# Optimization experiments

Hardware: AMD Instinct MI355X
Metric: run time of the kernel (lower is better)

## Reference

```python
import jax, jax.numpy as jnp
import numpy as np

COMMITMENT = 0.25
THRESHOLD = 0.6
SNR_DB = 30.0  # eval_snr_db default-ish channel condition (fixed for determinism)
LN_EPS = 1e-5


def _layernorm(x, g, b):
    m = jnp.mean(x, axis=-1, keepdims=True)
    v = jnp.var(x, axis=-1, keepdims=True)
    return (x - m) * jax.lax.rsqrt(v + LN_EPS) * g + b


def _vq(x, codebook):
    # x: [T, D], codebook: [K, D]. Nearest-neighbor quantize + per-token VQ loss + STE.
    d = (x * x).sum(-1, keepdims=True) - 2.0 * (x @ codebook.T) + (codebook * codebook).sum(-1)  # [T, K]
    idx = jnp.argmin(d, axis=-1)
    q = codebook[idx]  # [T, D]
    loss = (COMMITMENT * jnp.mean((x - jax.lax.stop_gradient(q)) ** 2, axis=-1)
            + jnp.mean((jax.lax.stop_gradient(x) - q) ** 2, axis=-1))  # [T]
    q_ste = x + jax.lax.stop_gradient(q - x)
    return q_ste, loss


def setup_inputs() -> dict:
    key = jax.random.key(0)
    ks = jax.random.split(key, 8)
    B, N, De, Dq, Dd = 64, 196, 768, 512, 256
    return {
        'x_tokens': jax.random.normal(ks[0], (B, N, De), jnp.float32),
        'fim_logits': jax.random.normal(ks[1], (B, N, 1), jnp.float32),
        'W_proj': jax.random.normal(ks[2], (De, Dq), jnp.float32) * (1.0 / np.sqrt(De)),
        'b_proj': jnp.zeros((Dq,), jnp.float32),
        'ln_g': jnp.ones((Dq,), jnp.float32),
        'ln_b': jnp.zeros((Dq,), jnp.float32),
        'cb_high': jax.random.normal(ks[3], (4096, Dq), jnp.float32),
        'cb_low': jax.random.normal(ks[4], (256, Dq), jnp.float32),
        'W_dec': jax.random.normal(ks[5], (Dq, Dd), jnp.float32) * (1.0 / np.sqrt(Dq)),
        'b_dec': jnp.zeros((Dd,), jnp.float32),
        'h_ri': jax.random.normal(ks[6], (B, 2), jnp.float32),
        'noise': jax.random.normal(ks[7], (B, N, Dq), jnp.float32),
    }


def reference(x_tokens, fim_logits, W_proj, b_proj, ln_g, ln_b, cb_high, cb_low, W_dec, b_dec, h_ri, noise):
    B, N, _ = x_tokens.shape
    score = jax.nn.sigmoid(fim_logits[..., 0])          # [B, N]
    route_high = score > THRESHOLD                       # [B, N] bool

    x_proj = _layernorm(x_tokens @ W_proj + b_proj, ln_g, ln_b)  # [B, N, Dq]
    D = x_proj.shape[-1]
    xf = x_proj.reshape(-1, D)
    mf = route_high.reshape(-1)
    sf = score.reshape(-1)

    # Compute both experts densely, select with mask (same math as the masked
    # gather/scatter dispatch in the torch code, jit-friendly static shapes).
    q_high, loss_high = _vq(xf, cb_high)
    q_low, loss_low = _vq(xf, cb_low)
    final = jnp.where(mf[:, None], q_high, q_low).reshape(B, N, D)

    n_high = jnp.maximum(mf.sum(), 1)
    n_low = jnp.maximum((~mf).sum(), 1)
    vq_loss = (jnp.sum(jnp.where(mf, loss_high * sf, 0.0)) / n_high
               + jnp.sum(jnp.where(mf, 0.0, loss_low * (1.0 - sf))) / n_low) / 2.0

    # Rayleigh channel: per-sample fading magnitude h = |CN(0,1)|/sqrt(2), AWGN, equalize.
    n_var = 10.0 ** (-SNR_DB / 10.0)
    h = jnp.sqrt((h_ri ** 2).sum(-1)) / jnp.sqrt(2.0)    # [B]
    h = h[:, None, None]
    y = (h * final + jnp.sqrt(n_var) * noise) / h

    x_dec = y @ W_dec + b_dec                            # [B, N, 256]
    return x_dec, vq_loss
```

## Files before the change

kernel.cpp:

```cpp
#include <hip/hip_runtime.h>
#include <math.h>

#define T_TOK 12544
#define DE 768
#define DQ 512
#define DD 256
#define SEQ 196
#define NCH 4096
#define NCL 256
#define SPL_H 16
#define CODES_PER_BLK 256
#define MARGIN 2.0f
#define CAND_CAP 16
#define VQTOK 128

typedef __attribute__((ext_vector_type(8))) short s16x8;
typedef __attribute__((ext_vector_type(4))) float f32x4;

__device__ __forceinline__ float wave_reduce_sum(float v) {
    #pragma unroll
    for (int off = 32; off > 0; off >>= 1) v += __shfl_xor(v, off);
    return v;
}

__device__ __forceinline__ unsigned short f2bf(float f) {
    unsigned int u = __float_as_uint(f);
    u = (u + 0x7fffu + ((u >> 16) & 1u)) >> 16;
    return (unsigned short)u;
}
__device__ __forceinline__ float bf2f(unsigned short h) {
    return __uint_as_float(((unsigned int)h) << 16);
}

__device__ __forceinline__ void gload_lds16(const unsigned short* g, unsigned short* l) {
    __builtin_amdgcn_global_load_lds(
        (const __attribute__((address_space(1))) void*)g,
        (__attribute__((address_space(3))) void*)l,
        16, 0, 0);
}

__device__ __forceinline__ void sumsq_body(const float* __restrict__ cb,
                                           float* __restrict__ cs2,
                                           unsigned short* __restrict__ cbB,
                                           int blk, int NC) {
    int row = blk * 4 + (threadIdx.x >> 6);
    int lane = threadIdx.x & 63;
    if (row >= NC) return;
    const float4* p = (const float4*)(cb + (size_t)row * DQ);
    float4 a = p[lane];
    float4 b = p[lane + 64];
    if (cbB) {
        unsigned short* dst = cbB + (size_t)row * DQ;
        ushort4 ha, hb;
        ha.x = f2bf(a.x); ha.y = f2bf(a.y); ha.z = f2bf(a.z); ha.w = f2bf(a.w);
        hb.x = f2bf(b.x); hb.y = f2bf(b.y); hb.z = f2bf(b.z); hb.w = f2bf(b.w);
        *(ushort4*)(dst + lane * 4) = ha;
        *(ushort4*)(dst + 256 + lane * 4) = hb;
    }
    float s = a.x*a.x + a.y*a.y + a.z*a.z + a.w*a.w
            + b.x*b.x + b.y*b.y + b.z*b.z + b.w*b.w;
    s = wave_reduce_sum(s);
    if (lane == 0) cs2[row] = s;
}

__device__ __forceinline__ void split_body(const float* __restrict__ W, int K, int N,
                                           unsigned short* __restrict__ Thi,
                                           unsigned short* __restrict__ Tlo,
                                           int blk, int nb) {
    int total = K * N;
    for (int idx = blk * 256 + threadIdx.x; idx < total; idx += nb * 256) {
        int n = idx / K, k = idx - n * K;
        float v = W[(size_t)k * N + n];
        unsigned short h = f2bf(v);
        Thi[idx] = h;
        Tlo[idx] = f2bf(v - bf2f(h));
    }
}

__global__ __launch_bounds__(256) void prep_all(const float* __restrict__ cb_h,
                                                float* __restrict__ cs2h,
                                                unsigned short* __restrict__ cbhB,
                                                const float* __restrict__ cb_l,
                                                float* __restrict__ cs2l,
                                                unsigned short* __restrict__ cblB,
                                                const float* __restrict__ Wp,
                                                unsigned short* __restrict__ WThi,
                                                unsigned short* __restrict__ WTlo,
                                                const float* __restrict__ Wd,
                                                unsigned short* __restrict__ WdThi,
                                                unsigned short* __restrict__ WdTlo,
                                                int* __restrict__ counts) {
    int blk = blockIdx.x;
    if (blk == 0 && threadIdx.x == 0) { counts[0] = 0; counts[1] = 0; }
    if (blk < 1024)       sumsq_body(cb_h, cs2h, cbhB, blk, NCH);
    else if (blk < 1088)  sumsq_body(cb_l, cs2l, cblB, blk - 1024, NCL);
    else if (blk < 1600)  split_body(Wp, DE, DQ, WThi, WTlo, blk - 1088, 512);
    else                  split_body(Wd, DQ, DD, WdThi, WdTlo, blk - 1600, 256);
}

template<int NC>
__global__ __launch_bounds__(256) void code_sumsq(const float* __restrict__ cb,
                                                  float* __restrict__ cs2) {
    sumsq_body(cb, cs2, nullptr, blockIdx.x, NC);
}

template<int KDIM, int NSTRIDE>
__global__ __launch_bounds__(256) void gemm_mfma3_128(const float* __restrict__ A,
                                                      const unsigned short* __restrict__ BThi,
                                                      const unsigned short* __restrict__ BTlo,
                                                      const float* __restrict__ bias,
                                                      float* __restrict__ out) {
    __shared__ __align__(16) unsigned short Ahi[128 * 32];
    __shared__ __align__(16) unsigned short Alo[128 * 32];
    __shared__ __align__(16) unsigned short Bhi[128 * 32];
    __shared__ __align__(16) unsigned short Blo[128 * 32];
    const int m0 = blockIdx.x * 128, n0 = blockIdx.y * 128;
    const int tid = threadIdx.x, lane = tid & 63, w = tid >> 6;
    const int wr = w >> 1, wc = w & 1;
    const int arow = tid >> 1, ahalf = tid & 1;

    const int cb0 = w * 2, cb1 = w * 2 + 1;
    const int gcol0 = n0 + cb0 * 16 + (lane >> 2);
    const int gcol1 = n0 + cb1 * 16 + (lane >> 2);
    const int ch0 = (lane & 3) ^ ((gcol0 >> 1) & 3);
    const int ch1 = (lane & 3) ^ ((gcol1 >> 1) & 3);
    const unsigned short* sH0 = BThi + (size_t)gcol0 * KDIM + ch0 * 8;
    const unsigned short* sH1 = BThi + (size_t)gcol1 * KDIM + ch1 * 8;
    const unsigned short* sL0 = BTlo + (size_t)gcol0 * KDIM + ch0 * 8;
    const unsigned short* sL1 = BTlo + (size_t)gcol1 * KDIM + ch1 * 8;

    f32x4 acc[4][4] = {};
    const int NT = KDIM / 32;
    for (int t = 0; t < NT; t++) {
        const int k0 = t * 32;
        gload_lds16(sH0 + k0, Bhi + cb0 * 512);
        gload_lds16(sH1 + k0, Bhi + cb1 * 512);
        gload_lds16(sL0 + k0, Blo + cb0 * 512);
        gload_lds16(sL1 + k0, Blo + cb1 * 512);
        {
            const float* src = A + (size_t)(m0 + arow) * KDIM + k0 + ahalf * 16;
            float4 v0 = *(const float4*)(src + 0);
            float4 v1 = *(const float4*)(src + 4);
            float4 v2 = *(const float4*)(src + 8);
            float4 v3 = *(const float4*)(src + 12);
            float xv[16] = {v0.x,v0.y,v0.z,v0.w, v1.x,v1.y,v1.z,v1.w,
                            v2.x,v2.y,v2.z,v2.w, v3.x,v3.y,v3.z,v3.w};
            const int swzA = (arow >> 1) & 3;
            #pragma unroll
            for (int cc = 0; cc < 2; cc++) {
                unsigned int hw[4], lw[4];
                #pragma unroll
                for (int j = 0; j < 4; j++) {
                    float f0 = xv[cc*8 + 2*j], f1 = xv[cc*8 + 2*j + 1];
                    unsigned short h0 = f2bf(f0), h1 = f2bf(f1);
                    unsigned short l0 = f2bf(f0 - bf2f(h0));
                    unsigned short l1 = f2bf(f1 - bf2f(h1));
                    hw[j] = (unsigned)h0 | ((unsigned)h1 << 16);
                    lw[j] = (unsigned)l0 | ((unsigned)l1 << 16);
                }
                int c = ahalf * 2 + cc;
                int doff = arow * 32 + (c ^ swzA) * 8;
                *(uint4*)&Ahi[doff] = make_uint4(hw[0], hw[1], hw[2], hw[3]);
                *(uint4*)&Alo[doff] = make_uint4(lw[0], lw[1], lw[2], lw[3]);
            }
        }
        __syncthreads();
        const int fr = lane & 15, fs = lane >> 4;
        s16x8 ah[4], al[4];
        #pragma unroll
        for (int tm = 0; tm < 4; tm++) {
            int row = wr * 64 + tm * 16 + fr;
            int off = row * 32 + (fs ^ ((row >> 1) & 3)) * 8;
            ah[tm] = *(const s16x8*)&Ahi[off];
            al[tm] = *(const s16x8*)&Alo[off];
        }
        #pragma unroll
        for (int tn = 0; tn < 4; tn++) {
            int col = wc * 64 + tn * 16 + fr;
            int boff = col * 32 + (fs ^ ((col >> 1) & 3)) * 8;
            s16x8 bh = *(const s16x8*)&Bhi[boff];
            s16x8 bl = *(const s16x8*)&Blo[boff];
            #pragma unroll
            for (int tm = 0; tm < 4; tm++) {
                acc[tm][tn] = __builtin_amdgcn_mfma_f32_16x16x32_bf16(ah[tm], bh, acc[tm][tn], 0, 0, 0);
                acc[tm][tn] = __builtin_amdgcn_mfma_f32_16x16x32_bf16(ah[tm], bl, acc[tm][tn], 0, 0, 0);
                acc[tm][tn] = __builtin_amdgcn_mfma_f32_16x16x32_bf16(al[tm], bh, acc[tm][tn], 0, 0, 0);
            }
        }
        __syncthreads();
    }
    const int fr = lane & 15, fg = lane >> 4;
    #pragma unroll
    for (int tn = 0; tn < 4; tn++) {
        const int col = n0 + wc * 64 + tn * 16 + fr;
        const float bb = bias[col];
        #pragma unroll
        for (int tm = 0; tm < 4; tm++) {
            #pragma unroll
            for (int r = 0; r < 4; r++) {
                int row = m0 + wr * 64 + tm * 16 + fg * 4 + r;
                out[(size_t)row * NSTRIDE + col] = acc[tm][tn][r] + bb;
            }
        }
    }
}

__global__ __launch_bounds__(256) void dec_mfma3_loss(const float* __restrict__ A,
                                                      const unsigned short* __restrict__ BThi,
                                                      const unsigned short* __restrict__ BTlo,
                                                      const float* __restrict__ bias,
                                                      float* __restrict__ out,
                                                      const float* __restrict__ lh,
                                                      const float* __restrict__ ll,
                                                      const int* __restrict__ counts) {
    __shared__ __align__(16) unsigned short Ahi[2][64 * 32];
    __shared__ __align__(16) unsigned short Alo[2][64 * 32];
    __shared__ __align__(16) unsigned short Bhi[2][64 * 32];
    __shared__ __align__(16) unsigned short Blo[2][64 * 32];
    if (blockIdx.x == T_TOK / 64) {
        if (blockIdx.y != 0) return;
        float* sh = (float*)&Ahi[0][0];
        float* sl = sh + 256;
        int tid = threadIdx.x;
        float ah = 0.f, al = 0.f;
        for (int t = tid; t < T_TOK; t += 256) { ah += lh[t]; al += ll[t]; }
        sh[tid] = ah; sl[tid] = al;
        __syncthreads();
        for (int o = 128; o > 0; o >>= 1) {
            if (tid < o) { sh[tid] += sh[tid + o]; sl[tid] += sl[tid + o]; }
            __syncthreads();
        }
        if (tid == 0) {
            int nh = counts[0];
            int nl = T_TOK - nh;
            nh = nh > 1 ? nh : 1;
            nl = nl > 1 ? nl : 1;
            out[(size_t)T_TOK * DD] = 0.5f * (sh[0] / (float)nh + sl[0] / (float)nl);
        }
        return;
    }
    const int m0 = blockIdx.x * 64, n0 = blockIdx.y * 64;
    const int tid = threadIdx.x, lane = tid & 63, w = tid >> 6;
    const int stok = tid >> 2, sslot = tid & 3;

    f32x4 acc[4] = {};
    float4 av0, av1;
    uint4 bh4, bl4;

    auto loadStep = [&](int k0) {
        const float* src = A + (size_t)(m0 + stok) * DQ + k0 + sslot * 8;
        av0 = *(const float4*)src;
        av1 = *(const float4*)(src + 4);
        size_t soff = (size_t)(n0 + stok) * DQ + k0 + sslot * 8;
        bh4 = *(const uint4*)(BThi + soff);
        bl4 = *(const uint4*)(BTlo + soff);
    };
    auto writeStep = [&](int buf) {
        float xv[8] = {av0.x, av0.y, av0.z, av0.w, av1.x, av1.y, av1.z, av1.w};
        unsigned int hw[4], lw[4];
        #pragma unroll
        for (int j = 0; j < 4; j++) {
            unsigned short h0 = f2bf(xv[2*j]),   h1 = f2bf(xv[2*j+1]);
            unsigned short l0 = f2bf(xv[2*j] - bf2f(h0));
            unsigned short l1 = f2bf(xv[2*j+1] - bf2f(h1));
            hw[j] = (unsigned)h0 | ((unsigned)h1 << 16);
            lw[j] = (unsigned)l0 | ((unsigned)l1 << 16);
        }
        int doffA = stok * 32 + (sslot ^ ((stok >> 1) & 3)) * 8;
        *(uint4*)&Ahi[buf][doffA] = make_uint4(hw[0], hw[1], hw[2], hw[3]);
        *(uint4*)&Alo[buf][doffA] = make_uint4(lw[0], lw[1], lw[2], lw[3]);
        *(uint4*)&Bhi[buf][doffA] = bh4;
        *(uint4*)&Blo[buf][doffA] = bl4;
    };

    loadStep(0); writeStep(0); __syncthreads();
    const int NT = DQ / 32;
    for (int t = 0; t < NT; t++) {
        const int cur = t & 1;
        if (t + 1 < NT) loadStep((t + 1) * 32);
        const int fr = lane & 15, fs = lane >> 4;
        s16x8 ah[4], al[4];
        #pragma unroll
        for (int tm = 0; tm < 4; tm++) {
            int tok = tm * 16 + fr;
            int off = tok * 32 + (fs ^ ((tok >> 1) & 3)) * 8;
            ah[tm] = *(const s16x8*)&Ahi[cur][off];
            al[tm] = *(const s16x8*)&Alo[cur][off];
        }
        {
            int col = w * 16 + fr;
            int boff = col * 32 + (fs ^ ((col >> 1) & 3)) * 8;
            s16x8 bh = *(const s16x8*)&Bhi[cur][boff];
            s16x8 bl = *(const s16x8*)&Blo[cur][boff];
            #pragma unroll
            for (int tm = 0; tm < 4; tm++) {
                acc[tm] = __builtin_amdgcn_mfma_f32_16x16x32_bf16(ah[tm], bh, acc[tm], 0, 0, 0);
                acc[tm] = __builtin_amdgcn_mfma_f32_16x16x32_bf16(ah[tm], bl, acc[tm], 0, 0, 0);
                acc[tm] = __builtin_amdgcn_mfma_f32_16x16x32_bf16(al[tm], bh, acc[tm], 0, 0, 0);
            }
        }
        if (t + 1 < NT) writeStep(cur ^ 1);
        __syncthreads();
    }
    const int fr = lane & 15, fg = lane >> 4;
    {
        const int col = n0 + w * 16 + fr;
        const float bb = bias[col];
        #pragma unroll
        for (int tm = 0; tm < 4; tm++) {
            #pragma unroll
            for (int r = 0; r < 4; r++) {
                int row = m0 + tm * 16 + fg * 4 + r;
                out[(size_t)row * DD + col] = acc[tm][r] + bb;
            }
        }
    }
}

__global__ __launch_bounds__(256) void proj_gemm(const float* __restrict__ X,
                                                 const float* __restrict__ W,
                                                 const float* __restrict__ bias,
                                                 float* __restrict__ out) {
    __shared__ float As[32][66];
    __shared__ float Bs[32][64];
    const int m0 = blockIdx.x * 64, n0 = blockIdx.y * 64;
    const int tid = threadIdx.x;
    const int tx = tid & 15, ty = tid >> 4;
    float acc[4][4] = {};
    for (int k0 = 0; k0 < DE; k0 += 32) {
        {
            int e = tid;
            int r = e >> 3, c4 = e & 7;
            float4 v = *(const float4*)(X + (size_t)(m0 + r) * DE + k0 + c4 * 4);
            As[c4*4+0][r] = v.x; As[c4*4+1][r] = v.y; As[c4*4+2][r] = v.z; As[c4*4+3][r] = v.w;
            e = tid + 256;
            r = e >> 3; c4 = e & 7;
            v = *(const float4*)(X + (size_t)(m0 + r) * DE + k0 + c4 * 4);
            As[c4*4+0][r] = v.x; As[c4*4+1][r] = v.y; As[c4*4+2][r] = v.z; As[c4*4+3][r] = v.w;
        }
        {
            int e = tid;
            int kk = e >> 4, c4 = e & 15;
            *(float4*)&Bs[kk][c4*4] = *(const float4*)(W + (size_t)(k0 + kk) * DQ + n0 + c4 * 4);
            e = tid + 256;
            kk = e >> 4; c4 = e & 15;
            *(float4*)&Bs[kk][c4*4] = *(const float4*)(W + (size_t)(k0 + kk) * DQ + n0 + c4 * 4);
        }
        __syncthreads();
        #pragma unroll
        for (int k = 0; k < 32; k++) {
            float2 a01 = *(const float2*)&As[k][ty * 4];
            float2 a23 = *(const float2*)&As[k][ty * 4 + 2];
            float4 b = *(const float4*)&Bs[k][tx * 4];
            float av[4] = {a01.x, a01.y, a23.x, a23.y};
            float bv[4] = {b.x, b.y, b.z, b.w};
            #pragma unroll
            for (int i = 0; i < 4; i++)
                #pragma unroll
                for (int j = 0; j < 4; j++)
                    acc[i][j] += av[i] * bv[j];
        }
        __syncthreads();
    }
    float4 bv4 = *(const float4*)(bias + n0 + tx * 4);
    float bb[4] = {bv4.x, bv4.y, bv4.z, bv4.w};
    #pragma unroll
    for (int i = 0; i < 4; i++) {
        int row = m0 + ty * 4 + i;
        float4 o;
        o.x = acc[i][0] + bb[0];
        o.y = acc[i][1] + bb[1];
        o.z = acc[i][2] + bb[2];
        o.w = acc[i][3] + bb[3];
        *(float4*)(out + (size_t)row * DQ + n0 + tx * 4) = o;
    }
}

__global__ __launch_bounds__(256) void ln_route_compact(float* __restrict__ xp,
                                                        const float* __restrict__ g,
                                                        const float* __restrict__ b,
                                                        const float* __restrict__ logits,
                                                        float* __restrict__ score,
                                                        unsigned short* __restrict__ xpB,
                                                        int* __restrict__ hlist,
                                                        int* __restrict__ llist,
                                                        int* __restrict__ counts) {
    __shared__ int hloc[32], lloc[32];
    __shared__ int nh_s, nl_s, bh_s, bl_s;
    const int tid = threadIdx.x, lane = tid & 63, wv = tid >> 6;
    if (tid == 0) { nh_s = 0; nl_s = 0; }
    __syncthreads();
    float4 g0 = *(const float4*)(g + lane * 4);
    float4 g1 = *(const float4*)(g + 256 + lane * 4);
    float4 b0 = *(const float4*)(b + lane * 4);
    float4 b1 = *(const float4*)(b + 256 + lane * 4);
    const int rbase = blockIdx.x * 32 + wv * 8;
    for (int i = 0; i < 8; i++) {
        int row = rbase + i;
        float* p = xp + (size_t)row * DQ;
        float4 v0 = *(float4*)(p + lane * 4);
        float4 v1 = *(float4*)(p + 256 + lane * 4);
        float s  = v0.x + v0.y + v0.z + v0.w + v1.x + v1.y + v1.z + v1.w;
        float ss = v0.x*v0.x + v0.y*v0.y + v0.z*v0.z + v0.w*v0.w
                 + v1.x*v1.x + v1.y*v1.y + v1.z*v1.z + v1.w*v1.w;
        s = wave_reduce_sum(s);
        ss = wave_reduce_sum(ss);
        float m = s * (1.f / DQ);
        float var = ss * (1.f / DQ) - m * m;
        float scale = rsqrtf(var + 1e-5f);
        float4 o0, o1;
        o0.x = (v0.x - m) * scale * g0.x + b0.x;
        o0.y = (v0.y - m) * scale * g0.y + b0.y;
        o0.z = (v0.z - m) * scale * g0.z + b0.z;
        o0.w = (v0.w - m) * scale * g0.w + b0.w;
        o1.x = (v1.x - m) * scale * g1.x + b1.x;
        o1.y = (v1.y - m) * scale * g1.y + b1.y;
        o1.z = (v1.z - m) * scale * g1.z + b1.z;
        o1.w = (v1.w - m) * scale * g1.w + b1.w;
        *(float4*)(p + lane * 4) = o0;
        *(float4*)(p + 256 + lane * 4) = o1;
        unsigned short* dst = xpB + (size_t)row * DQ;
        ushort4 h0, h1;
        h0.x = f2bf(o0.x); h0.y = f2bf(o0.y); h0.z = f2bf(o0.z); h0.w = f2bf(o0.w);
        h1.x = f2bf(o1.x); h1.y = f2bf(o1.y); h1.z = f2bf(o1.z); h1.w = f2bf(o1.w);
        *(ushort4*)(dst + lane * 4) = h0;
        *(ushort4*)(dst + 256 + lane * 4) = h1;
        if (lane == 0) {
            float lg = logits[row];
            float sc = 1.f / (1.f + expf(-lg));
            score[row] = sc;
            if (sc > 0.6f) { int pp = atomicAdd(&nh_s, 1); hloc[pp] = row; }
            else           { int pp = atomicAdd(&nl_s, 1); lloc[pp] = row; }
        }
    }
    __syncthreads();
    if (tid == 0) {
        bh_s = atomicAdd(&counts[0], nh_s);
        bl_s = atomicAdd(&counts[1], nl_s);
    }
    __syncthreads();
    if (tid < 32) {
        if (tid < nh_s) hlist[bh_s + tid] = hloc[tid];
    } else if (tid < 64) {
        int j = tid - 32;
        if (j < nl_s) llist[bl_s + j] = lloc[j];
    }
}

__global__ __launch_bounds__(256) void ln_route(float* __restrict__ xp,
                                                const float* __restrict__ g,
                                                const float* __restrict__ b,
                                                const float* __restrict__ logits,
                                                float* __restrict__ score,
                                                int* __restrict__ mask,
                                                unsigned short* __restrict__ xpB) {
    int row = blockIdx.x * 4 + (threadIdx.x >> 6);
    int lane = threadIdx.x & 63;
    float* p = xp + (size_t)row * DQ;
    float4 v0 = *(float4*)(p + lane * 4);
    float4 v1 = *(float4*)(p + 256 + lane * 4);
    float s  = v0.x + v0.y + v0.z + v0.w + v1.x + v1.y + v1.z + v1.w;
    float ss = v0.x*v0.x + v0.y*v0.y + v0.z*v0.z + v0.w*v0.w
             + v1.x*v1.x + v1.y*v1.y + v1.z*v1.z + v1.w*v1.w;
    s = wave_reduce_sum(s);
    ss = wave_reduce_sum(ss);
    float m = s * (1.f / DQ);
    float var = ss * (1.f / DQ) - m * m;
    float scale = rsqrtf(var + 1e-5f);
    float4 g0 = *(const float4*)(g + lane * 4);
    float4 g1 = *(const float4*)(g + 256 + lane * 4);
    float4 b0 = *(const float4*)(b + lane * 4);
    float4 b1 = *(const float4*)(b + 256 + lane * 4);
    float4 o0, o1;
    o0.x = (v0.x - m) * scale * g0.x + b0.x;
    o0.y = (v0.y - m) * scale * g0.y + b0.y;
    o0.z = (v0.z - m) * scale * g0.z + b0.z;
    o0.w = (v0.w - m) * scale * g0.w + b0.w;
    o1.x = (v1.x - m) * scale * g1.x + b1.x;
    o1.y = (v1.y - m) * scale * g1.y + b1.y;
    o1.z = (v1.z - m) * scale * g1.z + b1.z;
    o1.w = (v1.w - m) * scale * g1.w + b1.w;
    *(float4*)(p + lane * 4) = o0;
    *(float4*)(p + 256 + lane * 4) = o1;
    if (xpB) {
        unsigned short* dst = xpB + (size_t)row * DQ;
        ushort4 h0, h1;
        h0.x = f2bf(o0.x); h0.y = f2bf(o0.y); h0.z = f2bf(o0.z); h0.w = f2bf(o0.w);
        h1.x = f2bf(o1.x); h1.y = f2bf(o1.y); h1.z = f2bf(o1.z); h1.w = f2bf(o1.w);
        *(ushort4*)(dst + lane * 4) = h0;
        *(ushort4*)(dst + 256 + lane * 4) = h1;
    }
    if (lane == 0) {
        float lg = logits[row];
        float sc = 1.f / (1.f + expf(-lg));
        score[row] = sc;
        mask[row] = sc > 0.6f ? 1 : 0;
    }
}

__global__ __launch_bounds__(1024) void scan_compact(const int* __restrict__ mask,
                                                     int* __restrict__ hlist,
                                                     int* __restrict__ llist,
                                                     int* __restrict__ counts) {
    __shared__ int wsum[16];
    __shared__ int base_h, base_l;
    int tid = threadIdx.x, lane = tid & 63, wid = tid >> 6;
    if (tid == 0) { base_h = 0; base_l = 0; }
    __syncthreads();
    for (int t0 = 0; t0 < T_TOK; t0 += 1024) {
        int t = t0 + tid;
        int valid = t < T_TOK;
        int m = valid ? mask[t] : 0;
        unsigned long long bal = __ballot(m);
        int pre = __popcll(bal & ((1ull << lane) - 1ull));
        if (lane == 0) wsum[wid] = __popcll(bal);
        __syncthreads();
        int woff = 0;
        for (int w = 0; w < wid; w++) woff += wsum[w];
        int btot = 0;
        for (int w = 0; w < 16; w++) btot += wsum[w];
        int vcnt = T_TOK - t0; if (vcnt > 1024) vcnt = 1024;
        int bh = base_h, bl = base_l;
        if (valid) {
            if (m) hlist[bh + woff + pre] = t;
            else   llist[bl + (tid - (woff + pre))] = t;
        }
        __syncthreads();
        if (tid == 0) { base_h = bh + btot; base_l = bl + (vcnt - btot); }
        __syncthreads();
    }
    if (tid == 0) { counts[0] = base_h; counts[1] = base_l; }
}

__global__ __launch_bounds__(512) void vq_mfma_all(const unsigned short* __restrict__ xpB,
                                                   const unsigned short* __restrict__ cbhB,
                                                   const float* __restrict__ cs2h,
                                                   const int* __restrict__ hlist,
                                                   const unsigned short* __restrict__ cblB,
                                                   const float* __restrict__ cs2l,
                                                   const int* __restrict__ llist,
                                                   const int* __restrict__ counts,
                                                   float* __restrict__ smaxH,
                                                   int* __restrict__ scntH,
                                                   uint2* __restrict__ candH,
                                                   float* __restrict__ smaxL,
                                                   int* __restrict__ scntL,
                                                   uint2* __restrict__ candL) {
    const int by = blockIdx.y;
    const unsigned short* cbB; const float* cs2; const int* list;
    float* smax; int* scnt; uint2* cand;
    int count, slice, SPLIT;
    if (by < SPL_H) {
        cbB = cbhB; cs2 = cs2h; list = hlist; count = counts[0];
        slice = by; SPLIT = SPL_H; smax = smaxH; scnt = scntH; cand = candH;
    } else {
        cbB = cblB; cs2 = cs2l; list = llist; count = counts[1];
        slice = 0; SPLIT = 1; smax = smaxL; scnt = scntL; cand = candL;
    }
    const int base = blockIdx.x * VQTOK;
    if (base >= count) return;
    const int cbase = slice * CODES_PER_BLK;

    __shared__ __align__(16) unsigned short Abuf[VQTOK * 32];
    __shared__ __align__(16) unsigned short Bbuf[256 * 32];
    __shared__ float wmaxs[8][64];
    __shared__ float tokmax[VQTOK];
    __shared__ int ccnt[VQTOK];
    __shared__ uint2 cland[VQTOK][CAND_CAP];
    __shared__ int rows_s[VQTOK];

    const int tid = threadIdx.x;
    const int lane = tid & 63;
    const int w = tid >> 6;
    const int wr = w >> 2, wc = w & 3;
    const int stok = tid >> 2, sslot = tid & 3;

    if (tid < VQTOK) {
        int tl = base + tid;
        rows_s[tid] = list[tl < count ? tl : (count - 1)];
        ccnt[tid] = 0;
    }
    __syncthreads();

    const int swz = sslot ^ ((stok >> 1) & 3);
    const unsigned short* gA  = xpB + (size_t)rows_s[stok] * DQ + swz * 8;
    const unsigned short* gB0 = cbB + (size_t)(cbase + stok) * DQ + swz * 8;
    const unsigned short* gB1 = cbB + (size_t)(cbase + 128 + stok) * DQ + swz * 8;
    unsigned short* dA  = Abuf + w * 512;
    unsigned short* dB0 = Bbuf + w * 512;
    unsigned short* dB1 = Bbuf + 128 * 32 + w * 512;

    f32x4 acc[4][4] = {};

    const int NT = DQ / 32;
    for (int t = 0; t < NT; t++) {
        const int k0 = t * 32;
        gload_lds16(gA  + k0, dA);
        gload_lds16(gB0 + k0, dB0);
        gload_lds16(gB1 + k0, dB1);
        __syncthreads();
        const int fr = lane & 15, fs = lane >> 4;
        s16x8 af[4], bf[4];
        #pragma unroll
        for (int tm = 0; tm < 4; tm++) {
            int tok = wr * 64 + tm * 16 + fr;
            af[tm] = *(const s16x8*)&Abuf[tok * 32 + (fs ^ ((tok >> 1) & 3)) * 8];
        }
        #pragma unroll
        for (int tn = 0; tn < 4; tn++) {
            int cl = wc * 64 + tn * 16 + fr;
            bf[tn] = *(const s16x8*)&Bbuf[cl * 32 + (fs ^ ((cl >> 1) & 3)) * 8];
        }
        #pragma unroll
        for (int tm = 0; tm < 4; tm++)
            #pragma unroll
            for (int tn = 0; tn < 4; tn++)
                acc[tm][tn] = __builtin_amdgcn_mfma_f32_16x16x32_bf16(af[tm], bf[tn], acc[tm][tn], 0, 0, 0);
        __syncthreads();
    }

    const int fr = lane & 15, fg = lane >> 4;
    float c2[4];
    #pragma unroll
    for (int tn = 0; tn < 4; tn++) c2[tn] = 0.5f * cs2[cbase + wc * 64 + tn * 16 + fr];

    #pragma unroll
    for (int tm = 0; tm < 4; tm++) {
        #pragma unroll
        for (int r = 0; r < 4; r++) {
            float m4 = -3.0e38f;
            #pragma unroll
            for (int tn = 0; tn < 4; tn++) {
                float s = acc[tm][tn][r] - c2[tn];
                m4 = fmaxf(m4, s);
            }
            #pragma unroll
            for (int off = 1; off < 16; off <<= 1)
                m4 = fmaxf(m4, __shfl_xor(m4, off));
            if (fr == 0) wmaxs[w][tm * 16 + fg * 4 + r] = m4;
        }
    }
    __syncthreads();
    if (tid < VQTOK) {
        int wrt = tid >> 6, tlc = tid & 63;
        tokmax[tid] = fmaxf(fmaxf(wmaxs[wrt * 4 + 0][tlc], wmaxs[wrt * 4 + 1][tlc]),
                            fmaxf(wmaxs[wrt * 4 + 2][tlc], wmaxs[wrt * 4 + 3][tlc]));
    }
    __syncthreads();

    #pragma unroll
    for (int tm = 0; tm < 4; tm++) {
        #pragma unroll
        for (int r = 0; r < 4; r++) {
            int token = wr * 64 + tm * 16 + fg * 4 + r;
            float thr = tokmax[token] - MARGIN;
            #pragma unroll
            for (int tn = 0; tn < 4; tn++) {
                float s = acc[tm][tn][r] - c2[tn];
                if (s > thr) {
                    int pos = atomicAdd(&ccnt[token], 1);
                    if (pos < CAND_CAP) {
                        uint2 cd;
                        cd.x = __float_as_uint(s);
                        cd.y = (unsigned)(cbase + wc * 64 + tn * 16 + fr);
                        cland[token][pos] = cd;
                    }
                }
            }
        }
    }
    __syncthreads();

    if (tid < VQTOK) {
        int tl = base + tid;
        if (tl < count) {
            smax[(size_t)tl * SPLIT + slice] = tokmax[tid];
            scnt[(size_t)tl * SPLIT + slice] = min(ccnt[tid], CAND_CAP);
        }
    }
    for (int i = tid; i < VQTOK * CAND_CAP; i += 512) {
        int token = i >> 4, j = i & (CAND_CAP - 1);
        int tl = base + token;
        if (tl < count && j < min(ccnt[token], CAND_CAP))
            cand[((size_t)tl * SPLIT + slice) * CAND_CAP + j] = cland[token][j];
    }
}

__global__ __launch_bounds__(256) void vq_rescore_all(float* __restrict__ xp,
                                                      const float* __restrict__ cb_h,
                                                      const float* __restrict__ smaxH,
                                                      const int* __restrict__ scntH,
                                                      const uint2* __restrict__ candH,
                                                      const int* __restrict__ hlist,
                                                      const float* __restrict__ cb_l,
                                                      const float* __restrict__ smaxL,
                                                      const int* __restrict__ scntL,
                                                      const uint2* __restrict__ candL,
                                                      const int* __restrict__ llist,
                                                      const int* __restrict__ counts,
                                                      int* __restrict__ out_idx,
                                                      const float* __restrict__ noise,
                                                      const float* __restrict__ h_ri,
                                                      const float* __restrict__ score,
                                                      float* __restrict__ lh,
                                                      float* __restrict__ ll) {
    const int HB = T_TOK / 4;
    int bx = blockIdx.x;
    const float* cb; const float* smax; const int* scnt; const uint2* cand; const int* list;
    int count, SPLIT, cidx;
    if (bx < HB) {
        cb = cb_h; smax = smaxH; scnt = scntH; cand = candH; list = hlist;
        count = counts[0]; SPLIT = SPL_H; cidx = 0;
    } else {
        bx -= HB;
        cb = cb_l; smax = smaxL; scnt = scntL; cand = candL; list = llist;
        count = counts[1]; SPLIT = 1; cidx = 1;
    }
    const int wid = threadIdx.x >> 6;
    const int lane = threadIdx.x & 63;
    const int tl = bx * 4 + wid;
    if (tl >= count) return;

    float gm = -3.0e38f;
    if (lane < SPLIT) gm = smax[(size_t)tl * SPLIT + lane];
    #pragma unroll
    for (int off = 1; off < 64; off <<= 1)
        gm = fmaxf(gm, __shfl_xor(gm, off));
    const float thr = gm - MARGIN;

    const int t = list[tl];
    float xv[8];
    #pragma unroll
    for (int kk = 0; kk < 8; kk++) xv[kk] = xp[(size_t)t * DQ + lane * 8 + kk];

    double bs = -1.0e300;
    int bi = 0x7fffffff;
    for (int s = 0; s < SPLIT; s++) {
        int cn = scnt[(size_t)tl * SPLIT + s];
        for (int j = 0; j < cn; j++) {
            uint2 cd = cand[((size_t)tl * SPLIT + s) * CAND_CAP + j];
            float av = __uint_as_float(cd.x);
            if (av >= thr) {
                int code = (int)cd.y;
                const float* crow = cb + (size_t)code * DQ;
                double dot = 0.0, nrm = 0.0;
                #pragma unroll
                for (int kk = 0; kk < 8; kk++) {
                    double cv = (double)crow[lane * 8 + kk];
                    dot += (double)xv[kk] * cv;
                    nrm += cv * cv;
                }
                #pragma unroll
                for (int off = 1; off < 64; off <<= 1) {
                    dot += __shfl_xor(dot, off);
                    nrm += __shfl_xor(nrm, off);
                }
                double sc = dot - 0.5 * nrm;
                if (sc > bs || (sc == bs && code < bi)) { bs = sc; bi = code; }
            }
        }
    }
    const float* qrow = cb + (size_t)bi * DQ;
    float4 q0 = *(const float4*)(qrow + lane * 8);
    float4 q1 = *(const float4*)(qrow + lane * 8 + 4);
    const float* nz = noise + (size_t)t * DQ;
    float4 n0 = *(const float4*)(nz + lane * 8);
    float4 n1 = *(const float4*)(nz + lane * 8 + 4);
    float ds = 0.f, dx;
    dx = xv[0] - q0.x; ds += dx * dx;
    dx = xv[1] - q0.y; ds += dx * dx;
    dx = xv[2] - q0.z; ds += dx * dx;
    dx = xv[3] - q0.w; ds += dx * dx;
    dx = xv[4] - q1.x; ds += dx * dx;
    dx = xv[5] - q1.y; ds += dx * dx;
    dx = xv[6] - q1.z; ds += dx * dx;
    dx = xv[7] - q1.w; ds += dx * dx;
    ds = wave_reduce_sum(ds);
    int bbt = t / SEQ;
    float hh0 = h_ri[bbt * 2], hh1 = h_ri[bbt * 2 + 1];
    float hh = sqrtf((hh0 * hh0 + hh1 * hh1) * 0.5f);
    float cc = sqrtf(1e-3f) / hh;
    float4 y0, y1;
    y0.x = q0.x + cc * n0.x; y0.y = q0.y + cc * n0.y;
    y0.z = q0.z + cc * n0.z; y0.w = q0.w + cc * n0.w;
    y1.x = q1.x + cc * n1.x; y1.y = q1.y + cc * n1.y;
    y1.z = q1.z + cc * n1.z; y1.w = q1.w + cc * n1.w;
    *(float4*)(xp + (size_t)t * DQ + lane * 8) = y0;
    *(float4*)(xp + (size_t)t * DQ + lane * 8 + 4) = y1;
    if (lane == 0) {
        out_idx[t] = bi;
        float loss = 1.25f * ds * (1.f / DQ);
        float sc = score[t];
        if (cidx == 0) { lh[t] = loss * sc;  ll[t] = 0.f; }
        else           { lh[t] = 0.f;        ll[t] = loss * (1.f - sc); }
    }
}

template<int NC, int SPLIT>
__global__ __launch_bounds__(256) void vq_partial(const float* __restrict__ xp,
                                                  const float* __restrict__ cb,
                                                  const float* __restrict__ cs2,
                                                  const int* __restrict__ list,
                                                  const int* __restrict__ counts,
                                                  int cidx,
                                                  float* __restrict__ part_s,
                                                  int* __restrict__ part_i) {
    const int count = counts[cidx];
    const int base = blockIdx.x * 64;
    if (base >= count) return;
    const int CODES = NC / SPLIT;
    const int cbase = blockIdx.y * CODES;
    __shared__ float As[32][68];
    __shared__ float Cs[32][68];
    __shared__ int rows_s[64];
    const int tid = threadIdx.x;
    if (tid < 64) {
        int tl = base + tid;
        rows_s[tid] = list[tl < count ? tl : (count - 1)];
    }
    __syncthreads();
    const int tx = tid & 15, ty = tid >> 4;
    float best_s[4];
    int best_i[4];
    #pragma unroll
    for (int i = 0; i < 4; i++) { best_s[i] = -3.0e38f; best_i[i] = 0; }
    for (int c0 = cbase; c0 < cbase + CODES; c0 += 64) {
        float acc[4][4] = {};
        for (int k0 = 0; k0 < DQ; k0 += 32) {
            {
                int e = tid;
                int r = e >> 3, c4 = e & 7;
                float4 v = *(const float4*)(xp + (size_t)rows_s[r] * DQ + k0 + c4 * 4);
                As[c4*4+0][r] = v.x; As[c4*4+1][r] = v.y; As[c4*4+2][r] = v.z; As[c4*4+3][r] = v.w;
                e = tid + 256; r = e >> 3; c4 = e & 7;
                v = *(const float4*)(xp + (size_t)rows_s[r] * DQ + k0 + c4 * 4);
                As[c4*4+0][r] = v.x; As[c4*4+1][r] = v.y; As[c4*4+2][r] = v.z; As[c4*4+3][r] = v.w;
            }
            {
                int e = tid;
                int r = e >> 3, c4 = e & 7;
                float4 v = *(const float4*)(cb + (size_t)(c0 + r) * DQ + k0 + c4 * 4);
                Cs[c4*4+0][r] = v.x; Cs[c4*4+1][r] = v.y; Cs[c4*4+2][r] = v.z; Cs[c4*4+3][r] = v.w;
                e = tid + 256; r = e >> 3; c4 = e & 7;
                v = *(const float4*)(cb + (size_t)(c0 + r) * DQ + k0 + c4 * 4);
                Cs[c4*4+0][r] = v.x; Cs[c4*4+1][r] = v.y; Cs[c4*4+2][r] = v.z; Cs[c4*4+3][r] = v.w;
            }
            __syncthreads();
            #pragma unroll
            for (int k = 0; k < 32; k++) {
                float4 a = *(const float4*)&As[k][ty * 4];
                float4 b = *(const float4*)&Cs[k][tx * 4];
                float av[4] = {a.x, a.y, a.z, a.w};
                float bv[4] = {b.x, b.y, b.z, b.w};
                #pragma unroll
                for (int i = 0; i < 4; i++)
                    #pragma unroll
                    for (int j = 0; j < 4; j++)
                        acc[i][j] += av[i] * bv[j];
            }
            __syncthreads();
        }
        float4 c2v = *(const float4*)(cs2 + c0 + tx * 4);
        float c2[4] = {c2v.x, c2v.y, c2v.z, c2v.w};
        #pragma unroll
        for (int i = 0; i < 4; i++) {
            float s = acc[i][0] - 0.5f * c2[0];
            int bi = c0 + tx * 4;
            #pragma unroll
            for (int j = 1; j < 4; j++) {
                float sj = acc[i][j] - 0.5f * c2[j];
                if (sj > s) { s = sj; bi = c0 + tx * 4 + j; }
            }
            #pragma unroll
            for (int off = 1; off < 16; off <<= 1) {
                float os = __shfl_xor(s, off);
                int oi = __shfl_xor(bi, off);
                if (os > s || (os == s && oi < bi)) { s = os; bi = oi; }
            }
            if (s > best_s[i] || (s == best_s[i] && bi < best_i[i])) {
                best_s[i] = s; best_i[i] = bi;
            }
        }
    }
    if (tx == 0) {
        #pragma unroll
        for (int i = 0; i < 4; i++) {
            int tl = base + ty * 4 + i;
            if (tl < count) {
                part_s[(size_t)tl * SPLIT + blockIdx.y] = best_s[i];
                part_i[(size_t)tl * SPLIT + blockIdx.y] = best_i[i];
            }
        }
    }
}

template<int SPLIT>
__global__ __launch_bounds__(256) void vq_reduce(const float* __restrict__ part_s,
                                                 const int* __restrict__ part_i,
                                                 const int* __restrict__ list,
                                                 const int* __restrict__ counts,
                                                 int cidx,
                                                 int* __restrict__ out_idx) {
    int tl = blockIdx.x * 256 + threadIdx.x;
    if (tl >= counts[cidx]) return;
    float bs = part_s[(size_t)tl * SPLIT];
    int bi = part_i[(size_t)tl * SPLIT];
    #pragma unroll
    for (int s = 1; s < SPLIT; s++) {
        float v = part_s[(size_t)tl * SPLIT + s];
        int vi = part_i[(size_t)tl * SPLIT + s];
        if (v > bs || (v == bs && vi < bi)) { bs = v; bi = vi; }
    }
    out_idx[list[tl]] = bi;
}

__global__ __launch_bounds__(256) void gather_loss_y(float* __restrict__ xp,
                                                     const float* __restrict__ cb_h,
                                                     const float* __restrict__ cb_l,
                                                     const int* __restrict__ idx,
                                                     const float* __restrict__ score,
                                                     const int* __restrict__ mask,
                                                     const float* __restrict__ noise,
                                                     const float* __restrict__ h_ri,
                                                     float* __restrict__ lh,
                                                     float* __restrict__ ll) {
    int t = blockIdx.x * 4 + (threadIdx.x >> 6);
    int lane = threadIdx.x & 63;
    int m = mask[t];
    float sc = score[t];
    const float* q = (m ? cb_h : cb_l) + (size_t)idx[t] * DQ;
    float* x = xp + (size_t)t * DQ;
    const float* nz = noise + (size_t)t * DQ;
    int bb = t / SEQ;
    float h0 = h_ri[bb * 2], h1 = h_ri[bb * 2 + 1];
    float h = sqrtf((h0 * h0 + h1 * h1) * 0.5f);
    float c = sqrtf(1e-3f) / h;
    float4 xv0 = *(float4*)(x + lane * 4);
    float4 xv1 = *(float4*)(x + 256 + lane * 4);
    float4 qv0 = *(const float4*)(q + lane * 4);
    float4 qv1 = *(const float4*)(q + 256 + lane * 4);
    float4 nv0 = *(const float4*)(nz + lane * 4);
    float4 nv1 = *(const float4*)(nz + 256 + lane * 4);
    float dx, ds = 0.f;
    dx = xv0.x - qv0.x; ds += dx * dx;
    dx = xv0.y - qv0.y; ds += dx * dx;
    dx = xv0.z - qv0.z; ds += dx * dx;
    dx = xv0.w - qv0.w; ds += dx * dx;
    dx = xv1.x - qv1.x; ds += dx * dx;
    dx = xv1.y - qv1.y; ds += dx * dx;
    dx = xv1.z - qv1.z; ds += dx * dx;
    dx = xv1.w - qv1.w; ds += dx * dx;
    ds = wave_reduce_sum(ds);
    float4 y0, y1;
    y0.x = qv0.x + c * nv0.x; y0.y = qv0.y + c * nv0.y;
    y0.z = qv0.z + c * nv0.z; y0.w = qv0.w + c * nv0.w;
    y1.x = qv1.x + c * nv1.x; y1.y = qv1.y + c * nv1.y;
    y1.z = qv1.z + c * nv1.z; y1.w = qv1.w + c * nv1.w;
    *(float4*)(x + lane * 4) = y0;
    *(float4*)(x + 256 + lane * 4) = y1;
    if (lane == 0) {
        float loss = 1.25f * ds * (1.f / DQ);
        lh[t] = m ? loss * sc : 0.f;
        ll[t] = m ? 0.f : loss * (1.f - sc);
    }
}

__global__ __launch_bounds__(256) void loss_reduce(const float* __restrict__ lh,
                                                   const float* __restrict__ ll,
                                                   const int* __restrict__ counts,
                                                   float* __restrict__ out) {
    __shared__ float sh[256], sl[256];
    int tid = threadIdx.x;
    float ah = 0.f, al = 0.f;
    for (int t = tid; t < T_TOK; t += 256) { ah += lh[t]; al += ll[t]; }
    sh[tid] = ah; sl[tid] = al;
    __syncthreads();
    for (int o = 128; o > 0; o >>= 1) {
        if (tid < o) { sh[tid] += sh[tid + o]; sl[tid] += sl[tid + o]; }
        __syncthreads();
    }
    if (tid == 0) {
        int nh = counts[0];
        int nl = T_TOK - nh;
        nh = nh > 1 ? nh : 1;
        nl = nl > 1 ? nl : 1;
        out[(size_t)T_TOK * DD] = 0.5f * (sh[0] / (float)nh + sl[0] / (float)nl);
    }
}

__global__ __launch_bounds__(256) void dec_gemm(const float* __restrict__ Y,
                                                const float* __restrict__ W,
                                                const float* __restrict__ bias,
                                                float* __restrict__ out) {
    __shared__ float As[32][66];
    __shared__ float Bs[32][64];
    const int m0 = blockIdx.x * 64, n0 = blockIdx.y * 64;
    const int tid = threadIdx.x;
    const int tx = tid & 15, ty = tid >> 4;
    float acc[4][4] = {};
    for (int k0 = 0; k0 < DQ; k0 += 32) {
        {
            int e = tid;
            int r = e >> 3, c4 = e & 7;
            float4 v = *(const float4*)(Y + (size_t)(m0 + r) * DQ + k0 + c4 * 4);
            As[c4*4+0][r] = v.x; As[c4*4+1][r] = v.y; As[c4*4+2][r] = v.z; As[c4*4+3][r] = v.w;
            e = tid + 256; r = e >> 3; c4 = e & 7;
            v = *(const float4*)(Y + (size_t)(m0 + r) * DQ + k0 + c4 * 4);
            As[c4*4+0][r] = v.x; As[c4*4+1][r] = v.y; As[c4*4+2][r] = v.z; As[c4*4+3][r] = v.w;
        }
        {
            int e = tid;
            int kk = e >> 4, c4 = e & 15;
            *(float4*)&Bs[kk][c4*4] = *(const float4*)(W + (size_t)(k0 + kk) * DD + n0 + c4 * 4);
            e = tid + 256; kk = e >> 4; c4 = e & 15;
            *(float4*)&Bs[kk][c4*4] = *(const float4*)(W + (size_t)(k0 + kk) * DD + n0 + c4 * 4);
        }
        __syncthreads();
        #pragma unroll
        for (int k = 0; k < 32; k++) {
            float2 a01 = *(const float2*)&As[k][ty * 4];
            float2 a23 = *(const float2*)&As[k][ty * 4 + 2];
            float4 b = *(const float4*)&Bs[k][tx * 4];
            float av[4] = {a01.x, a01.y, a23.x, a23.y};
            float bv[4] = {b.x, b.y, b.z, b.w};
            #pragma unroll
            for (int i = 0; i < 4; i++)
                #pragma unroll
                for (int j = 0; j < 4; j++)
                    acc[i][j] += av[i] * bv[j];
        }
        __syncthreads();
    }
    float4 bv4 = *(const float4*)(bias + n0 + tx * 4);
    float bbv[4] = {bv4.x, bv4.y, bv4.z, bv4.w};
    #pragma unroll
    for (int i = 0; i < 4; i++) {
        int row = m0 + ty * 4 + i;
        float4 o;
        o.x = acc[i][0] + bbv[0];
        o.y = acc[i][1] + bbv[1];
        o.z = acc[i][2] + bbv[2];
        o.w = acc[i][3] + bbv[3];
        *(float4*)(out + (size_t)row * DD + n0 + tx * 4) = o;
    }
}

extern "C" void kernel_launch(void* const* d_in, const int* in_sizes, int n_in,
                              void* d_out, int out_size, void* d_ws, size_t ws_size,
                              hipStream_t stream) {
    const float* x_tokens = (const float*)d_in[0];
    const float* fim      = (const float*)d_in[1];
    const float* W_proj   = (const float*)d_in[2];
    const float* b_proj   = (const float*)d_in[3];
    const float* ln_g     = (const float*)d_in[4];
    const float* ln_b     = (const float*)d_in[5];
    const float* cb_high  = (const float*)d_in[6];
    const float* cb_low   = (const float*)d_in[7];
    const float* W_dec    = (const float*)d_in[8];
    const float* b_dec    = (const float*)d_in[9];
    const float* h_ri     = (const float*)d_in[10];
    const float* noise    = (const float*)d_in[11];
    float* out = (float*)d_out;

    char* ws = (char*)d_ws;
    size_t off = 0;
    float* xp = (float*)(ws + off);     off += (size_t)T_TOK * DQ * 4;
    int*   idxb = (int*)(ws + off);     off += (size_t)T_TOK * 4;
    float* score = (float*)(ws + off);  off += (size_t)T_TOK * 4;
    int*   mask = (int*)(ws + off);     off += (size_t)T_TOK * 4;
    float* lh = (float*)(ws + off);     off += (size_t)T_TOK * 4;
    float* ll = (float*)(ws + off);     off += (size_t)T_TOK * 4;
    int*   hlist = (int*)(ws + off);    off += (size_t)T_TOK * 4;
    int*   llist = (int*)(ws + off);    off += (size_t)T_TOK * 4;
    int*   counts = (int*)(ws + off);   off += 64;
    float* cs2h = (float*)(ws + off);   off += (size_t)NCH * 4;
    float* cs2l = (float*)(ws + off);   off += (size_t)NCL * 4;
    size_t off_common = off;

    unsigned short* xpB  = (unsigned short*)(ws + off); off += (size_t)T_TOK * DQ * 2;
    unsigned short* cbhB = (unsigned short*)(ws + off); off += (size_t)NCH * DQ * 2;
    unsigned short* cblB = (unsigned short*)(ws + off); off += (size_t)NCL * DQ * 2;
    float* smaxH = (float*)(ws + off);  off += (size_t)T_TOK * SPL_H * 4;
    int*   scntH = (int*)(ws + off);    off += (size_t)T_TOK * SPL_H * 4;
    uint2* candH = (uint2*)(ws + off);  off += (size_t)T_TOK * SPL_H * CAND_CAP * 8;
    float* smaxL = (float*)(ws + off);  off += (size_t)T_TOK * 4;
    int*   scntL = (int*)(ws + off);    off += (size_t)T_TOK * 4;
    uint2* candL = (uint2*)(ws + off);  off += (size_t)T_TOK * CAND_CAP * 8;
    unsigned short* WThi  = (unsigned short*)(ws + off); off += (size_t)DQ * DE * 2;
    unsigned short* WTlo  = (unsigned short*)(ws + off); off += (size_t)DQ * DE * 2;
    unsigned short* WdThi = (unsigned short*)(ws + off); off += (size_t)DD * DQ * 2;
    unsigned short* WdTlo = (unsigned short*)(ws + off); off += (size_t)DD * DQ * 2;
    size_t need_new = off;
    const bool use_mfma = ws_size >= need_new;

    if (use_mfma) {
        prep_all<<<1856, 256, 0, stream>>>(cb_high, cs2h, cbhB, cb_low, cs2l, cblB,
                                           W_proj, WThi, WTlo, W_dec, WdThi, WdTlo, counts);
        gemm_mfma3_128<DE, DQ><<<dim3(T_TOK / 128, DQ / 128), 256, 0, stream>>>(
            x_tokens, WThi, WTlo, b_proj, xp);
        ln_route_compact<<<T_TOK / 32, 256, 0, stream>>>(
            xp, ln_g, ln_b, fim, score, xpB, hlist, llist, counts);
        vq_mfma_all<<<dim3(T_TOK / VQTOK, SPL_H + 1), 512, 0, stream>>>(
            xpB, cbhB, cs2h, hlist, cblB, cs2l, llist, counts,
            smaxH, scntH, candH, smaxL, scntL, candL);
        vq_rescore_all<<<2 * (T_TOK / 4), 256, 0, stream>>>(
            xp, cb_high, smaxH, scntH, candH, hlist,
            cb_low, smaxL, scntL, candL, llist,
            counts, idxb, noise, h_ri, score, lh, ll);
        dec_mfma3_loss<<<dim3(T_TOK / 64 + 1, DD / 64), 256, 0, stream>>>(
            xp, WdThi, WdTlo, b_dec, out, lh, ll, counts);
    } else {
        code_sumsq<NCH><<<NCH / 4, 256, 0, stream>>>(cb_high, cs2h);
        code_sumsq<NCL><<<NCL / 4, 256, 0, stream>>>(cb_low, cs2l);
        proj_gemm<<<dim3(T_TOK / 64, DQ / 64), 256, 0, stream>>>(x_tokens, W_proj, b_proj, xp);
        ln_route<<<T_TOK / 4, 256, 0, stream>>>(xp, ln_g, ln_b, fim, score, mask, nullptr);
        scan_compact<<<1, 1024, 0, stream>>>(mask, hlist, llist, counts);
        float* part_s = (float*)(ws + off_common);
        int*   part_i = (int*)(ws + off_common + (size_t)T_TOK * 16 * 4);
        vq_partial<NCH, 16><<<dim3(T_TOK / 64, 16), 256, 0, stream>>>(
            xp, cb_high, cs2h, hlist, counts, 0, part_s, part_i);
        vq_reduce<16><<<(T_TOK + 255) / 256, 256, 0, stream>>>(part_s, part_i, hlist, counts, 0, idxb);
        vq_partial<NCL, 4><<<dim3(T_TOK / 64, 4), 256, 0, stream>>>(
            xp, cb_low, cs2l, llist, counts, 1, part_s, part_i);
        vq_reduce<4><<<(T_TOK + 255) / 256, 256, 0, stream>>>(part_s, part_i, llist, counts, 1, idxb);
        gather_loss_y<<<T_TOK / 4, 256, 0, stream>>>(xp, cb_high, cb_low, idxb, score, mask,
                                                     noise, h_ri, lh, ll);
        loss_reduce<<<1, 256, 0, stream>>>(lh, ll, counts, out);
        dec_gemm<<<dim3(T_TOK / 64, DD / 64), 256, 0, stream>>>(xp, W_dec, b_dec, out);
    }
}
```

Measured before the change: 198.0 us.

## Triple-buffer VQ distance GEMM with async LDS loads and union shared memory

```diff
diff --git a/kernel.cpp b/kernel.cpp
--- a/kernel.cpp
+++ b/kernel.cpp
@@ -283,7 +283,9 @@
         #pragma unroll
         for (int tm = 0; tm < 4; tm++) {
             int tok = tm * 16 + fr;
-            int off = tok * 32 + (fs ^ ((tok >> 1) & 3)) * 8;
+            int off = tok * 32 + (sslot, fs ^ ((tok >> 1) & 3)) * 8;
+            (void)off;
+            off = tok * 32 + (fs ^ ((tok >> 1) & 3)) * 8;
             ah[tm] = *(const s16x8*)&Ahi[cur][off];
             al[tm] = *(const s16x8*)&Alo[cur][off];
         }
@@ -561,13 +563,12 @@
     if (base >= count) return;
     const int cbase = slice * CODES_PER_BLK;
 
-    __shared__ __align__(16) unsigned short Abuf[VQTOK * 32];
-    __shared__ __align__(16) unsigned short Bbuf[256 * 32];
-    __shared__ float wmaxs[8][64];
-    __shared__ float tokmax[VQTOK];
-    __shared__ int ccnt[VQTOK];
-    __shared__ uint2 cland[VQTOK][CAND_CAP];
-    __shared__ int rows_s[VQTOK];
+    __shared__ __align__(16) unsigned char SMEM[3 * 24576 + 512];
+    int* rows_s = (int*)(SMEM + 3 * 24576);
+    uint2 (*cland)[CAND_CAP] = (uint2(*)[CAND_CAP])SMEM;
+    float* wmaxs  = (float*)(SMEM + 16384);
+    float* tokmax = (float*)(SMEM + 18432);
+    int*   ccnt   = (int*)(SMEM + 18944);
 
     const int tid = threadIdx.x;
     const int lane = tid & 63;
@@ -578,7 +579,6 @@
     if (tid < VQTOK) {
         int tl = base + tid;
         rows_s[tid] = list[tl < count ? tl : (count - 1)];
-        ccnt[tid] = 0;
     }
     __syncthreads();
 
@@ -586,43 +586,62 @@
     const unsigned short* gA  = xpB + (size_t)rows_s[stok] * DQ + swz * 8;
     const unsigned short* gB0 = cbB + (size_t)(cbase + stok) * DQ + swz * 8;
     const unsigned short* gB1 = cbB + (size_t)(cbase + 128 + stok) * DQ + swz * 8;
-    unsigned short* dA  = Abuf + w * 512;
-    unsigned short* dB0 = Bbuf + w * 512;
-    unsigned short* dB1 = Bbuf + 128 * 32 + w * 512;
+
+    auto stage = [&](int buf, int k0) {
+        unsigned short* Ab = (unsigned short*)(SMEM + buf * 24576);
+        gload_lds16(gA  + k0, Ab + w * 512);
+        gload_lds16(gB0 + k0, Ab + 4096 + w * 512);
+        gload_lds16(gB1 + k0, Ab + 8192 + w * 512);
+    };
 
     f32x4 acc[4][4] = {};
-
-    const int NT = DQ / 32;
-    for (int t = 0; t < NT; t++) {
-        const int k0 = t * 32;
-        gload_lds16(gA  + k0, dA);
-        gload_lds16(gB0 + k0, dB0);
-        gload_lds16(gB1 + k0, dB1);
-        __syncthreads();
-        const int fr = lane & 15, fs = lane >> 4;
+    const int fr = lane & 15, fs = lane >> 4;
+
+    auto compute = [&](int buf) {
+        const unsigned short* Ab = (const unsigned short*)(SMEM + buf * 24576);
+        const unsigned short* Bb = Ab + 4096;
         s16x8 af[4], bf[4];
         #pragma unroll
         for (int tm = 0; tm < 4; tm++) {
             int tok = wr * 64 + tm * 16 + fr;
-            af[tm] = *(const s16x8*)&Abuf[tok * 32 + (fs ^ ((tok >> 1) & 3)) * 8];
+            af[tm] = *(const s16x8*)&Ab[tok * 32 + (fs ^ ((tok >> 1) & 3)) * 8];
         }
         #pragma unroll
         for (int tn = 0; tn < 4; tn++) {
             int cl = wc * 64 + tn * 16 + fr;
-            bf[tn] = *(const s16x8*)&Bbuf[cl * 32 + (fs ^ ((cl >> 1) & 3)) * 8];
+            bf[tn] = *(const s16x8*)&Bb[cl * 32 + (fs ^ ((cl >> 1) & 3)) * 8];
         }
         #pragma unroll
         for (int tm = 0; tm < 4; tm++)
             #pragma unroll
             for (int tn = 0; tn < 4; tn++)
                 acc[tm][tn] = __builtin_amdgcn_mfma_f32_16x16x32_bf16(af[tm], bf[tn], acc[tm][tn], 0, 0, 0);
-        __syncthreads();
-    }
-
-    const int fr = lane & 15, fg = lane >> 4;
+    };
+
+    stage(0, 0);
+    stage(1, 32);
+    for (int t = 0; t < 14; t++) {
+        asm volatile("s_waitcnt vmcnt(3)" ::: "memory");
+        __builtin_amdgcn_s_barrier();
+        __builtin_amdgcn_sched_barrier(0);
+        stage((t + 2) % 3, (t + 2) * 32);
+        compute(t % 3);
+    }
+    asm volatile("s_waitcnt vmcnt(3)" ::: "memory");
+    __builtin_amdgcn_s_barrier();
+    __builtin_amdgcn_sched_barrier(0);
+    compute(14 % 3);
+    asm volatile("s_waitcnt vmcnt(0)" ::: "memory");
+    __builtin_amdgcn_s_barrier();
+    __builtin_amdgcn_sched_barrier(0);
+    compute(15 % 3);
+    __syncthreads();
+
+    if (tid < VQTOK) ccnt[tid] = 0;
     float c2[4];
     #pragma unroll
     for (int tn = 0; tn < 4; tn++) c2[tn] = 0.5f * cs2[cbase + wc * 64 + tn * 16 + fr];
+    const int fg = lane >> 4;
 
     #pragma unroll
     for (int tm = 0; tm < 4; tm++) {
@@ -637,14 +656,14 @@
             #pragma unroll
             for (int off = 1; off < 16; off <<= 1)
                 m4 = fmaxf(m4, __shfl_xor(m4, off));
-            if (fr == 0) wmaxs[w][tm * 16 + fg * 4 + r] = m4;
+            if (fr == 0) wmaxs[w * 64 + tm * 16 + fg * 4 + r] = m4;
         }
     }
     __syncthreads();
     if (tid < VQTOK) {
         int wrt = tid >> 6, tlc = tid & 63;
-        tokmax[tid] = fmaxf(fmaxf(wmaxs[wrt * 4 + 0][tlc], wmaxs[wrt * 4 + 1][tlc]),
-                            fmaxf(wmaxs[wrt * 4 + 2][tlc], wmaxs[wrt * 4 + 3][tlc]));
+        tokmax[tid] = fmaxf(fmaxf(wmaxs[(wrt * 4 + 0) * 64 + tlc], wmaxs[(wrt * 4 + 1) * 64 + tlc]),
+                            fmaxf(wmaxs[(wrt * 4 + 2) * 64 + tlc], wmaxs[(wrt * 4 + 3) * 64 + tlc]));
     }
     __syncthreads();
 
```

After: 183.3 us. 7.4% less time.
